# Kernel tuning notes

Hardware: AMD Instinct MI355X
Metric: run time of the kernel (lower is better)

The kernel has to match this reference:

```python
import jax, jax.numpy as jnp
import numpy as np

EPS = 1e-5
NUM_HEADS = 16
TEMP = 0.01

def _ln(x, g, b):
    m = jnp.mean(x, axis=-1, keepdims=True)
    v = jnp.var(x, axis=-1, keepdims=True)
    return (x - m) * jax.lax.rsqrt(v + EPS) * g + b

def setup_inputs() -> dict:
    key = jax.random.key(0)
    ks = jax.random.split(key, 16)
    b, l, c, ni = 4, 1024, 1024, 2
    d = c // NUM_HEADS
    s = lambda fan: 1.0 / np.sqrt(fan)
    return {
        "x_list": jax.random.normal(ks[0], (b, l, c, ni), jnp.float32),
        "w_": jax.random.normal(ks[1], (4 + ni, 1), jnp.float32),
        "qkv_w": jax.random.normal(ks[2], (3 * c, c), jnp.float32) * s(c),
        "qkv_b": jax.random.normal(ks[3], (3 * c,), jnp.float32) * 0.02,
        "proj_w": jax.random.normal(ks[4], (c, c), jnp.float32) * s(c),
        "proj_b": jax.random.normal(ks[5], (c,), jnp.float32) * 0.02,
        "nq_g": jnp.ones((d,), jnp.float32),
        "nq_b": jnp.zeros((d,), jnp.float32),
        "nk_g": jnp.ones((d,), jnp.float32),
        "nk_b": jnp.zeros((d,), jnp.float32),
        "conv_w": jax.random.normal(ks[6], (c, c), jnp.float32) * s(c),
        "conv_b": jax.random.normal(ks[7], (c,), jnp.float32) * 0.02,
        "ca1_w": jax.random.normal(ks[8], (c // 16, c), jnp.float32) * s(c),
        "ca1_b": jax.random.normal(ks[9], (c // 16,), jnp.float32) * 0.02,
        "ca2_w": jax.random.normal(ks[10], (c, c // 16), jnp.float32) * s(c // 16),
        "ca2_b": jax.random.normal(ks[11], (c,), jnp.float32) * 0.02,
        "mlp1_w": jax.random.normal(ks[12], (4 * c, c), jnp.float32) * s(c),
        "mlp1_b": jax.random.normal(ks[13], (4 * c,), jnp.float32) * 0.02,
        "mlp2_w": jax.random.normal(ks[14], (c, 4 * c), jnp.float32) * s(4 * c),
        "mlp2_b": jax.random.normal(ks[15], (c,), jnp.float32) * 0.02,
    }

def reference(x_list, w_, qkv_w, qkv_b, proj_w, proj_b, nq_g, nq_b, nk_g, nk_b,
              conv_w, conv_b, ca1_w, ca1_b, ca2_w, ca2_b, mlp1_w, mlp1_b, mlp2_w, mlp2_b):
    x = x_list[..., -1]  # [b, l, c]
    # op 0: Conv1x1Act = GELU(Linear)
    op0 = jax.nn.gelu(x @ conv_w.T + conv_b, approximate=False)
    # op 1: ChannelAttention = sigmoid(fc2(relu(fc1(x)))) * x
    op1 = jax.nn.sigmoid(jax.nn.relu(x @ ca1_w.T + ca1_b) @ ca2_w.T + ca2_b) * x
    # op 2: Identity
    op2 = x
    # op 3: MLP = fc2(GELU(fc1(x)))
    op3 = jax.nn.gelu(x @ mlp1_w.T + mlp1_b, approximate=False) @ mlp2_w.T + mlp2_b
    new = jnp.stack([op0, op1, op2, op3], axis=-1)  # [b, l, c, 4]
    xc = jnp.concatenate([x_list, new], axis=-1)    # [b, l, c, ni+4]
    w = jax.nn.softmax(w_ / TEMP, axis=0)           # [ni+4, 1]
    x = jnp.einsum('blcn,ni->blci', xc, w)[..., 0]  # [b, l, c]
    x_res = x
    # attention with per-head LayerNorm on q, k
    b_, n, c = x.shape
    d = c // NUM_HEADS
    qkv = x @ qkv_w.T + qkv_b
    q, k, v = jnp.split(qkv, 3, axis=-1)
    to_heads = lambda t: t.reshape(b_, n, NUM_HEADS, d).transpose(0, 2, 1, 3)  # [b, h, n, d]
    q, k, v = to_heads(q), to_heads(k), to_heads(v)
    q = _ln(q, nq_g, nq_b)
    k = _ln(k, nk_g, nk_b)
    score = jnp.einsum('bhnd,bhmd->bhnm', q, k) / np.sqrt(d).astype(np.float32)
    attn = jax.nn.softmax(score, axis=-1)           # [b, h, n, n]
    attn_map = attn.mean(axis=1)[:, 0, 1:]          # [b, n-1]
    out = jnp.einsum('bhnm,bhmd->bhnd', attn, v)
    out = out.transpose(0, 2, 1, 3).reshape(b_, n, c)
    out = out @ proj_w.T + proj_b + x_res
    return out, attn_map
```

## Files before the change

kernel.cpp:

```cpp
#include <hip/hip_runtime.h>
#include <hip/hip_bf16.h>

typedef __attribute__((ext_vector_type(8))) short short8;
typedef __attribute__((ext_vector_type(4))) float f32x4;

#define MROWS 4096
#define CDIM  1024
#define HEADS 16
#define DHEAD 64
#define NSEQ  1024

__device__ inline float softw(const float* __restrict__ w, int idx) {
    float m = w[0];
#pragma unroll
    for (int i = 1; i < 6; i++) m = fmaxf(m, w[i]);
    float s = 0.f, v = 0.f;
#pragma unroll
    for (int i = 0; i < 6; i++) {
        float e = __expf((w[i] - m) * 100.0f);
        s += e;
        if (i == idx) v = e;
    }
    return v / s;
}

__device__ inline float gelu_f(float x) {
    return 0.5f * x * (1.0f + erff(x * 0.70710678118654752f));
}

__global__ __launch_bounds__(256) void mix_base(
    const float* __restrict__ x_list, __hip_bfloat16* __restrict__ xb,
    float* __restrict__ am_acc)
{
    int i = blockIdx.x * 256 + threadIdx.x;
    xb[i] = __float2bfloat16(x_list[2 * (size_t)i + 1]);
    if (i < 4096) am_acc[i] = 0.f;
}

__global__ __launch_bounds__(256) void f2b(const float* __restrict__ in,
                                           __hip_bfloat16* __restrict__ out, int n)
{
    int i = blockIdx.x * 256 + threadIdx.x;
    if (i < n) out[i] = __float2bfloat16(in[i]);
}

#define BKT 32
#define LDA 40

template<int EPI, int FM, int FN>
__global__ __launch_bounds__(256) void gemm_bf16(
    const __hip_bfloat16* __restrict__ A, const __hip_bfloat16* __restrict__ W,
    const float* __restrict__ bias,
    float* __restrict__ f0, const float* __restrict__ f1,
    __hip_bfloat16* __restrict__ b0, __hip_bfloat16* __restrict__ b1,
    __hip_bfloat16* __restrict__ b2,
    const float* __restrict__ g0, const float* __restrict__ be0,
    const float* __restrict__ g1, const float* __restrict__ be1,
    const float* __restrict__ wvec, int M, int N, int K)
{
    constexpr int BMt = FM * 32;
    constexpr int BNt = FN * 32;
    constexpr int NA = BMt / 64;
    constexpr int NB = BNt / 64;
    __shared__ __hip_bfloat16 As[2][BMt * LDA];
    __shared__ __hip_bfloat16 Bs[2][BNt * LDA];
    int t = threadIdx.x;
    int n0 = blockIdx.x * BNt, m0 = blockIdx.y * BMt;
    int wave = t >> 6, lane = t & 63;
    int wr = wave >> 1, wc = wave & 1;
    int quad = lane >> 4, l16 = lane & 15;
    int r0 = t >> 2, c0 = (t & 3) * 8;

    short8 sa0[NA], sb0[NB], sa1[NA], sb1[NB];
    auto ldg = [&](int k0, short8* da, short8* db) {
#pragma unroll
        for (int i = 0; i < NA; i++)
            da[i] = *(const short8*)(A + (size_t)(m0 + r0 + 64 * i) * K + k0 + c0);
#pragma unroll
        for (int i = 0; i < NB; i++)
            db[i] = *(const short8*)(W + (size_t)(n0 + r0 + 64 * i) * K + k0 + c0);
    };
    ldg(0, sa0, sb0);
    ldg(BKT, sa1, sb1);

    f32x4 zero = {0.f, 0.f, 0.f, 0.f};
    f32x4 acc[FM][FN];
#pragma unroll
    for (int i = 0; i < FM; i++)
#pragma unroll
        for (int j = 0; j < FN; j++) acc[i][j] = zero;

    for (int k0 = 0; k0 < K; k0 += 2 * BKT) {
#pragma unroll
        for (int i = 0; i < NA; i++)
            *(short8*)&As[0][(r0 + 64 * i) * LDA + c0] = sa0[i];
#pragma unroll
        for (int i = 0; i < NB; i++)
            *(short8*)&Bs[0][(r0 + 64 * i) * LDA + c0] = sb0[i];
        __syncthreads();
        if (k0 + 2 * BKT < K) ldg(k0 + 2 * BKT, sa0, sb0);
        {
            short8 af[FM], bf[FN];
#pragma unroll
            for (int i = 0; i < FM; i++)
                af[i] = *(const short8*)&As[0][(wr * FM * 16 + i * 16 + l16) * LDA + quad * 8];
#pragma unroll
            for (int j = 0; j < FN; j++)
                bf[j] = *(const short8*)&Bs[0][(wc * FN * 16 + j * 16 + l16) * LDA + quad * 8];
#pragma unroll
            for (int i = 0; i < FM; i++)
#pragma unroll
                for (int j = 0; j < FN; j++)
                    acc[i][j] = __builtin_amdgcn_mfma_f32_16x16x32_bf16(
                        af[i], bf[j], acc[i][j], 0, 0, 0);
        }
#pragma unroll
        for (int i = 0; i < NA; i++)
            *(short8*)&As[1][(r0 + 64 * i) * LDA + c0] = sa1[i];
#pragma unroll
        for (int i = 0; i < NB; i++)
            *(short8*)&Bs[1][(r0 + 64 * i) * LDA + c0] = sb1[i];
        __syncthreads();
        if (k0 + 3 * BKT < K) ldg(k0 + 3 * BKT, sa1, sb1);
        {
            short8 af[FM], bf[FN];
#pragma unroll
            for (int i = 0; i < FM; i++)
                af[i] = *(const short8*)&As[1][(wr * FM * 16 + i * 16 + l16) * LDA + quad * 8];
#pragma unroll
            for (int j = 0; j < FN; j++)
                bf[j] = *(const short8*)&Bs[1][(wc * FN * 16 + j * 16 + l16) * LDA + quad * 8];
#pragma unroll
            for (int i = 0; i < FM; i++)
#pragma unroll
                for (int j = 0; j < FN; j++)
                    acc[i][j] = __builtin_amdgcn_mfma_f32_16x16x32_bf16(
                        af[i], bf[j], acc[i][j], 0, 0, 0);
        }
    }

    if constexpr (EPI == 1) {
        float wmx = softw(wvec, 2);
        float w0c = softw(wvec, 0);
        float w14c = softw(wvec, 1) + softw(wvec, 4);
        int colbase = n0 + wc * FN * 16;
        bool isconv = colbase < 1024;
#pragma unroll
        for (int i = 0; i < FM; i++) {
#pragma unroll
            for (int j = 0; j < FN; j++) {
                int col = colbase + j * 16 + l16;
                float bv = isconv ? bias[col] : be0[col - 1024];
#pragma unroll
                for (int r = 0; r < 4; r++) {
                    int row = m0 + wr * FM * 16 + i * 16 + quad * 4 + r;
                    float v = acc[i][j][r] + bv;
                    if (isconv) {
                        size_t idx = (size_t)row * 1024 + col;
                        float2 xl = ((const float2*)f1)[idx];
                        b0[idx] = __float2bfloat16(
                            w0c * xl.x + w14c * xl.y + wmx * gelu_f(v));
                    } else {
                        b1[(size_t)row * 4096 + (col - 1024)] =
                            __float2bfloat16(gelu_f(v));
                    }
                }
            }
        }
        return;
    }

    if constexpr (EPI == 5) {
        int colbase = n0 + wc * FN * 16;
        int portion = colbase >> 10;
        int hh = (colbase >> 6) & 15;
        float bv[FN];
#pragma unroll
        for (int j = 0; j < FN; j++) bv[j] = bias[colbase + j * 16 + l16];
        if (portion == 2) {
#pragma unroll
            for (int i = 0; i < FM; i++)
#pragma unroll
                for (int j = 0; j < FN; j++)
#pragma unroll
                    for (int r = 0; r < 4; r++) {
                        int row = m0 + wr * FM * 16 + i * 16 + quad * 4 + r;
                        int bb = row >> 10, nn = row & 1023;
                        int dd = j * 16 + l16;
                        b0[((size_t)(bb * 16 + hh) * DHEAD + dd) * NSEQ + nn] =
                            __float2bfloat16(acc[i][j][r] + bv[j]);
                    }
        } else {
            const float* g  = (portion == 0) ? g0 : g1;
            const float* be = (portion == 0) ? be0 : be1;
            __hip_bfloat16* dst = (portion == 0) ? b1 : b2;
            float gv[FN], bev[FN];
#pragma unroll
            for (int j = 0; j < FN; j++) {
                gv[j] = g[j * 16 + l16];
                bev[j] = be[j * 16 + l16];
            }
#pragma unroll
            for (int i = 0; i < FM; i++)
#pragma unroll
                for (int r = 0; r < 4; r++) {
                    float s1 = 0.f, s2 = 0.f;
#pragma unroll
                    for (int j = 0; j < FN; j++) {
                        float v = acc[i][j][r] + bv[j];
                        s1 += v; s2 += v * v;
                    }
#pragma unroll
                    for (int mk = 1; mk < 16; mk <<= 1) {
                        s1 += __shfl_xor(s1, mk, 64);
                        s2 += __shfl_xor(s2, mk, 64);
                    }
                    float mean = s1 * (1.f / 64.f);
                    float var = s2 * (1.f / 64.f) - mean * mean;
                    float rs = rsqrtf(var + 1e-5f);
                    int row = m0 + wr * FM * 16 + i * 16 + quad * 4 + r;
                    int bb = row >> 10, nn = row & 1023;
                    size_t base = ((size_t)(bb * 16 + hh) * NSEQ + nn) * DHEAD;
#pragma unroll
                    for (int j = 0; j < FN; j++)
                        dst[base + j * 16 + l16] = __float2bfloat16(
                            (acc[i][j][r] + bv[j] - mean) * rs * gv[j] + bev[j]);
                }
        }
        return;
    }

    float wmx = 0.f;
    if (EPI == 3) wmx = softw(wvec, 5);

#pragma unroll
    for (int i = 0; i < FM; i++) {
#pragma unroll
        for (int j = 0; j < FN; j++) {
            int col = n0 + wc * FN * 16 + j * 16 + l16;
            float bv = bias[col];
#pragma unroll
            for (int r = 0; r < 4; r++) {
                int row = m0 + wr * FM * 16 + i * 16 + quad * 4 + r;
                float v = acc[i][j][r] + bv;
                size_t idx = (size_t)row * N + col;
                if (EPI == 3) {
                    float tv = __bfloat162float(b0[idx]) + wmx * v;
                    b0[idx] = __float2bfloat16(tv);
                } else if (EPI == 4) {
                    f0[idx] = v + __bfloat162float(b1[idx]);
                }
            }
        }
    }
}

__global__ __launch_bounds__(256) void ca1_kernel(
    const __hip_bfloat16* __restrict__ xb, const float* __restrict__ w,
    const float* __restrict__ bias, float* __restrict__ h1)
{
    __shared__ float Xs[16 * 65];
    __shared__ float Ws[64 * 65];
    int t = threadIdx.x;
    int m0 = blockIdx.x * 16;
    int row = t >> 4, cg = t & 15;
    float acc[4] = {0.f, 0.f, 0.f, 0.f};
    for (int k0 = 0; k0 < 1024; k0 += 64) {
#pragma unroll
        for (int i = 0; i < 4; i++) {
            int e = t + i * 256; int r = e >> 6, c = e & 63;
            Xs[r * 65 + c] = __bfloat162float(xb[(size_t)(m0 + r) * 1024 + k0 + c]);
        }
#pragma unroll
        for (int i = 0; i < 16; i++) {
            int e = t + i * 256; int r = e >> 6, c = e & 63;
            Ws[r * 65 + c] = w[(size_t)r * 1024 + k0 + c];
        }
        __syncthreads();
        for (int k = 0; k < 64; k++) {
            float xv = Xs[row * 65 + k];
#pragma unroll
            for (int c = 0; c < 4; c++)
                acc[c] += xv * Ws[(cg * 4 + c) * 65 + k];
        }
        __syncthreads();
    }
#pragma unroll
    for (int c = 0; c < 4; c++)
        h1[(size_t)(m0 + row) * 64 + cg * 4 + c] =
            fmaxf(acc[c] + bias[cg * 4 + c], 0.f);
}

__global__ __launch_bounds__(256) void ca2_kernel(
    const float* __restrict__ h1, const float* __restrict__ w,
    const float* __restrict__ bias, const __hip_bfloat16* __restrict__ xb,
    __hip_bfloat16* __restrict__ xmixb, const float* __restrict__ wvec)
{
    __shared__ float Wt[256 * 65];
    __shared__ float hs[16 * 64];
    int t = threadIdx.x;
    int m0 = blockIdx.x * 16, n0 = blockIdx.y * 256;
#pragma unroll
    for (int i = 0; i < 64; i++) {
        int e = t + i * 256; int r = e >> 6, c = e & 63;
        Wt[r * 65 + c] = w[(size_t)(n0 + r) * 64 + c];
    }
#pragma unroll
    for (int i = 0; i < 4; i++) {
        int e = t + i * 256; int r = e >> 6, c = e & 63;
        hs[r * 64 + c] = h1[(size_t)(m0 + r) * 64 + c];
    }
    __syncthreads();
    int n = n0 + t;
    float bv = bias[n];
    float acc[16];
#pragma unroll
    for (int mi = 0; mi < 16; mi++) acc[mi] = bv;
    for (int k = 0; k < 64; k++) {
        float wv = Wt[t * 65 + k];
#pragma unroll
        for (int mi = 0; mi < 16; mi++) acc[mi] += hs[mi * 64 + k] * wv;
    }
    float w3 = softw(wvec, 3);
#pragma unroll
    for (int mi = 0; mi < 16; mi++) {
        size_t idx = (size_t)(m0 + mi) * 1024 + n;
        float sg = 1.f / (1.f + __expf(-acc[mi]));
        float cur = __bfloat162float(xmixb[idx]);
        xmixb[idx] = __float2bfloat16(cur + w3 * sg * __bfloat162float(xb[idx]));
    }
}

#define PSTR 72
__global__ __launch_bounds__(256) void flash_mfma(
    const __hip_bfloat16* __restrict__ qb, const __hip_bfloat16* __restrict__ kb,
    const __hip_bfloat16* __restrict__ vt, __hip_bfloat16* __restrict__ ao)
{
    __shared__ __hip_bfloat16 Plds[4][32 * PSTR];
    int bh = blockIdx.x;
    int i0 = blockIdx.y * 128;
    int b = bh >> 4, h = bh & 15;
    int t = threadIdx.x, wave = t >> 6, lane = t & 63;
    int l16 = lane & 15, quad = lane >> 4;
    const __hip_bfloat16* qbase = qb + (size_t)bh * NSEQ * DHEAD;
    const __hip_bfloat16* kbase = kb + (size_t)bh * NSEQ * DHEAD;
    const __hip_bfloat16* vbase = vt + (size_t)bh * DHEAD * NSEQ;
    __hip_bfloat16* pw = Plds[wave];
    int qrow0 = i0 + wave * 32;

    short8 aq[2][2];
#pragma unroll
    for (int ri = 0; ri < 2; ri++)
#pragma unroll
        for (int ks = 0; ks < 2; ks++)
            aq[ri][ks] = *(const short8*)(qbase +
                (size_t)(qrow0 + ri * 16 + l16) * DHEAD + ks * 32 + quad * 8);

    f32x4 zero = {0.f, 0.f, 0.f, 0.f};
    f32x4 o[2][4];
    float mrow[2][4], lrow[2][4];
#pragma unroll
    for (int ri = 0; ri < 2; ri++) {
#pragma unroll
        for (int nt = 0; nt < 4; nt++) o[ri][nt] = zero;
#pragma unroll
        for (int rr = 0; rr < 4; rr++) { mrow[ri][rr] = -1e30f; lrow[ri][rr] = 0.f; }
    }

    for (int j0 = 0; j0 < NSEQ; j0 += 64) {
        short8 bk[4][2];
#pragma unroll
        for (int jt = 0; jt < 4; jt++)
#pragma unroll
            for (int ks = 0; ks < 2; ks++)
                bk[jt][ks] = *(const short8*)(kbase +
                    (size_t)(j0 + jt * 16 + l16) * DHEAD + ks * 32 + quad * 8);
        short8 bv[4][2];
#pragma unroll
        for (int nt = 0; nt < 4; nt++)
#pragma unroll
            for (int ks = 0; ks < 2; ks++)
                bv[nt][ks] = *(const short8*)(vbase +
                    (size_t)(nt * 16 + l16) * NSEQ + j0 + ks * 32 + quad * 8);

#pragma unroll
        for (int ri = 0; ri < 2; ri++) {
            f32x4 s[4];
#pragma unroll
            for (int jt = 0; jt < 4; jt++) s[jt] = zero;
#pragma unroll
            for (int jt = 0; jt < 4; jt++)
#pragma unroll
                for (int ks = 0; ks < 2; ks++)
                    s[jt] = __builtin_amdgcn_mfma_f32_16x16x32_bf16(
                        aq[ri][ks], bk[jt][ks], s[jt], 0, 0, 0);
#pragma unroll
            for (int rr = 0; rr < 4; rr++) {
                float mx = -1e30f;
#pragma unroll
                for (int jt = 0; jt < 4; jt++) {
                    s[jt][rr] *= 0.125f;
                    mx = fmaxf(mx, s[jt][rr]);
                }
#pragma unroll
                for (int mk = 1; mk < 16; mk <<= 1) mx = fmaxf(mx, __shfl_xor(mx, mk, 64));
                float om = mrow[ri][rr];
                float nm = fmaxf(om, mx);
                float al = __expf(om - nm);
                mrow[ri][rr] = nm;
                float ss = 0.f;
#pragma unroll
                for (int jt = 0; jt < 4; jt++) {
                    float p = __expf(s[jt][rr] - nm);
                    pw[(ri * 16 + quad * 4 + rr) * PSTR + jt * 16 + l16] =
                        __float2bfloat16(p);
                    ss += p;
                }
#pragma unroll
                for (int mk = 1; mk < 16; mk <<= 1) ss += __shfl_xor(ss, mk, 64);
                lrow[ri][rr] = lrow[ri][rr] * al + ss;
#pragma unroll
                for (int nt = 0; nt < 4; nt++) o[ri][nt][rr] *= al;
            }
        }
#pragma unroll
        for (int ri = 0; ri < 2; ri++) {
            short8 ap[2];
#pragma unroll
            for (int ks = 0; ks < 2; ks++)
                ap[ks] = *(const short8*)&pw[(ri * 16 + l16) * PSTR + ks * 32 + quad * 8];
#pragma unroll
            for (int nt = 0; nt < 4; nt++)
#pragma unroll
                for (int ks = 0; ks < 2; ks++)
                    o[ri][nt] = __builtin_amdgcn_mfma_f32_16x16x32_bf16(
                        ap[ks], bv[nt][ks], o[ri][nt], 0, 0, 0);
        }
    }

#pragma unroll
    for (int ri = 0; ri < 2; ri++)
#pragma unroll
        for (int rr = 0; rr < 4; rr++) {
            float inv = 1.f / lrow[ri][rr];
            int row = qrow0 + ri * 16 + quad * 4 + rr;
#pragma unroll
            for (int nt = 0; nt < 4; nt++)
                ao[((size_t)b * NSEQ + row) * CDIM + h * 64 + nt * 16 + l16] =
                    __float2bfloat16(o[ri][nt][rr] * inv);
        }
}

__global__ __launch_bounds__(256) void attn_map_acc(
    const __hip_bfloat16* __restrict__ qf, const __hip_bfloat16* __restrict__ kf,
    float* __restrict__ am)
{
    __shared__ float q0[64];
    __shared__ float red[256];
    int bh = blockIdx.x, t = threadIdx.x;
    const __hip_bfloat16* qr = qf + (size_t)bh * NSEQ * DHEAD;
    const __hip_bfloat16* kb = kf + (size_t)bh * NSEQ * DHEAD;
    if (t < 64) q0[t] = __bfloat162float(qr[t]);
    __syncthreads();
    float s[4];
    float mx = -1e30f;
#pragma unroll
    for (int ji = 0; ji < 4; ji++) {
        int j = ji * 256 + t;
        float a = 0.f;
        for (int k = 0; k < 64; k++) a += q0[k] * __bfloat162float(kb[(size_t)j * 64 + k]);
        a *= 0.125f;
        s[ji] = a;
        mx = fmaxf(mx, a);
    }
    red[t] = mx; __syncthreads();
    for (int st = 128; st > 0; st >>= 1) {
        if (t < st) red[t] = fmaxf(red[t], red[t + st]);
        __syncthreads();
    }
    float M = red[0]; __syncthreads();
    float sum = 0.f;
#pragma unroll
    for (int ji = 0; ji < 4; ji++) { s[ji] = __expf(s[ji] - M); sum += s[ji]; }
    red[t] = sum; __syncthreads();
    for (int st = 128; st > 0; st >>= 1) {
        if (t < st) red[t] += red[t + st];
        __syncthreads();
    }
    float inv = 1.f / red[0];
    int b = bh >> 4;
#pragma unroll
    for (int ji = 0; ji < 4; ji++) {
        int j = ji * 256 + t;
        if (j > 0) atomicAdd(&am[b * 1024 + j], s[ji] * inv * (1.f / 16.f));
    }
}

__global__ __launch_bounds__(256) void attn_map_out(
    const float* __restrict__ am, float* __restrict__ out1)
{
    int i = blockIdx.x * 256 + threadIdx.x;
    if (i < 4 * 1023) {
        int b = i / 1023;
        int j = i - b * 1023 + 1;
        out1[i] = am[b * 1024 + j];
    }
}

extern "C" void kernel_launch(void* const* d_in, const int* in_sizes, int n_in,
                              void* d_out, int out_size, void* d_ws, size_t ws_size,
                              hipStream_t stream)
{
    const float* x_list = (const float*)d_in[0];
    const float* wvec   = (const float*)d_in[1];
    const float* qkv_w  = (const float*)d_in[2];
    const float* qkv_b  = (const float*)d_in[3];
    const float* proj_w = (const float*)d_in[4];
    const float* proj_b = (const float*)d_in[5];
    const float* nq_g   = (const float*)d_in[6];
    const float* nq_b   = (const float*)d_in[7];
    const float* nk_g   = (const float*)d_in[8];
    const float* nk_b   = (const float*)d_in[9];
    const float* conv_w = (const float*)d_in[10];
    const float* conv_b = (const float*)d_in[11];
    const float* ca1_w  = (const float*)d_in[12];
    const float* ca1_b  = (const float*)d_in[13];
    const float* ca2_w  = (const float*)d_in[14];
    const float* ca2_b  = (const float*)d_in[15];
    const float* mlp1_w = (const float*)d_in[16];
    const float* mlp1_b = (const float*)d_in[17];
    const float* mlp2_w = (const float*)d_in[18];
    const float* mlp2_b = (const float*)d_in[19];

    float* out0 = (float*)d_out;
    float* out1 = out0 + (size_t)4 * 1024 * 1024;

    char* ws = (char*)d_ws;
    size_t off = 0;
    auto alloc = [&](size_t bytes) -> char* {
        char* p = ws + off;
        off += (bytes + 255) & ~(size_t)255;
        return p;
    };
    __hip_bfloat16* xb     = (__hip_bfloat16*)alloc((size_t)MROWS * CDIM * 2);
    __hip_bfloat16* xmixb  = (__hip_bfloat16*)alloc((size_t)MROWS * CDIM * 2);
    float*          h1     = (float*)alloc((size_t)MROWS * 64 * 4);
    __hip_bfloat16* hb     = (__hip_bfloat16*)alloc((size_t)MROWS * 4096 * 2);
    __hip_bfloat16* qbb    = (__hip_bfloat16*)alloc((size_t)MROWS * CDIM * 2);
    __hip_bfloat16* kbb    = (__hip_bfloat16*)alloc((size_t)MROWS * CDIM * 2);
    __hip_bfloat16* vtb    = (__hip_bfloat16*)alloc((size_t)MROWS * CDIM * 2);
    __hip_bfloat16* aob    = (__hip_bfloat16*)alloc((size_t)MROWS * CDIM * 2);
    float*          amacc  = (float*)alloc(4096 * 4);
    __hip_bfloat16* wcat   = (__hip_bfloat16*)alloc((size_t)5120 * 1024 * 2);
    __hip_bfloat16* qkvwb  = (__hip_bfloat16*)alloc((size_t)3145728 * 2);
    __hip_bfloat16* projwb = (__hip_bfloat16*)alloc((size_t)1048576 * 2);
    __hip_bfloat16* mlp2wb = (__hip_bfloat16*)alloc((size_t)4194304 * 2);

    f2b<<<4096, 256, 0, stream>>>(conv_w, wcat, 1048576);
    f2b<<<16384, 256, 0, stream>>>(mlp1_w, wcat + (size_t)1048576, 4194304);
    f2b<<<12288, 256, 0, stream>>>(qkv_w, qkvwb, 3145728);
    f2b<<<4096, 256, 0, stream>>>(proj_w, projwb, 1048576);
    f2b<<<16384, 256, 0, stream>>>(mlp2_w, mlp2wb, 4194304);

    mix_base<<<16384, 256, 0, stream>>>(x_list, xb, amacc);

    gemm_bf16<1, 4, 4><<<dim3(40, 32), 256, 0, stream>>>(
        xb, wcat, conv_b, nullptr, x_list, xmixb, hb, nullptr,
        nullptr, mlp1_b, nullptr, nullptr, wvec, MROWS, 5120, 1024);

    ca1_kernel<<<256, 256, 0, stream>>>(xb, ca1_w, ca1_b, h1);
    ca2_kernel<<<dim3(256, 4), 256, 0, stream>>>(h1, ca2_w, ca2_b, xb, xmixb, wvec);

    gemm_bf16<3, 4, 4><<<dim3(8, 32), 256, 0, stream>>>(
        hb, mlp2wb, mlp2_b, nullptr, nullptr, xmixb, nullptr, nullptr,
        nullptr, nullptr, nullptr, nullptr, wvec, MROWS, 1024, 4096);

    gemm_bf16<5, 4, 4><<<dim3(24, 32), 256, 0, stream>>>(
        xmixb, qkvwb, qkv_b, nullptr, nullptr, vtb, qbb, kbb,
        nq_g, nq_b, nk_g, nk_b, wvec, MROWS, 3072, 1024);

    flash_mfma<<<dim3(64, 8), 256, 0, stream>>>(qbb, kbb, vtb, aob);

    attn_map_acc<<<64, 256, 0, stream>>>(qbb, kbb, amacc);
    attn_map_out<<<16, 256, 0, stream>>>(amacc, out1);

    gemm_bf16<4, 4, 4><<<dim3(8, 32), 256, 0, stream>>>(
        aob, projwb, proj_b, out0, nullptr, nullptr, xmixb, nullptr,
        nullptr, nullptr, nullptr, nullptr, wvec, MROWS, 1024, 1024);
}
```

Before: 549.6 us.

## Add 256x256 direct-to-LDS GEMM for fused conv/mlp1 and QKV; merge weight casts

Adds a new 512-thread GEMM kernel with 256x256 tiles that loads A and B straight into a 4-stage shared-memory ring via global_load_lds. It uses swizzled addressing, XCD-aware block remapping, split barriers and MFMA priority hints. It replaces the 128x128 GEMM for the conv+mlp1 and QKV projections. It also merges the five weight-cast launches into one vectorized kernel and vectorizes the input extraction. The aim is more data reuse per tile, fewer launches and better load/compute overlap. The cost is heavy register and LDS use, with only 320 or 192 blocks, so fewer blocks are available to fill the CUs.

```diff
diff --git a/kernel.cpp b/kernel.cpp
--- a/kernel.cpp
+++ b/kernel.cpp
@@ -32,16 +32,35 @@
     const float* __restrict__ x_list, __hip_bfloat16* __restrict__ xb,
     float* __restrict__ am_acc)
 {
-    int i = blockIdx.x * 256 + threadIdx.x;
-    xb[i] = __float2bfloat16(x_list[2 * (size_t)i + 1]);
-    if (i < 4096) am_acc[i] = 0.f;
-}
-
-__global__ __launch_bounds__(256) void f2b(const float* __restrict__ in,
-                                           __hip_bfloat16* __restrict__ out, int n)
-{
-    int i = blockIdx.x * 256 + threadIdx.x;
-    if (i < n) out[i] = __float2bfloat16(in[i]);
+    int i2 = blockIdx.x * 256 + threadIdx.x;
+    float4 v = ((const float4*)x_list)[i2];
+    __hip_bfloat162 o;
+    o.x = __float2bfloat16(v.y);
+    o.y = __float2bfloat16(v.w);
+    ((__hip_bfloat162*)xb)[i2] = o;
+    if (i2 < 4096) am_acc[i2] = 0.f;
+}
+
+__global__ __launch_bounds__(256) void f2b_all(
+    const float* __restrict__ conv_w, const float* __restrict__ mlp1_w,
+    const float* __restrict__ qkv_w, const float* __restrict__ proj_w,
+    const float* __restrict__ mlp2_w,
+    __hip_bfloat16* __restrict__ wcat, __hip_bfloat16* __restrict__ qkvwb,
+    __hip_bfloat16* __restrict__ projwb, __hip_bfloat16* __restrict__ mlp2wb)
+{
+    size_t e = ((size_t)blockIdx.x * 256 + threadIdx.x) * 4;
+    const float* src; __hip_bfloat16* dst; size_t o;
+    if (e < 1048576)       { src = conv_w; dst = wcat;           o = e; }
+    else if (e < 5242880)  { src = mlp1_w; dst = wcat + 1048576; o = e - 1048576; }
+    else if (e < 8388608)  { src = qkv_w;  dst = qkvwb;          o = e - 5242880; }
+    else if (e < 9437184)  { src = proj_w; dst = projwb;         o = e - 8388608; }
+    else                   { src = mlp2_w; dst = mlp2wb;         o = e - 9437184; }
+    float4 v = *(const float4*)(src + o);
+    __hip_bfloat162 a, b;
+    a.x = __float2bfloat16(v.x); a.y = __float2bfloat16(v.y);
+    b.x = __float2bfloat16(v.z); b.y = __float2bfloat16(v.w);
+    *(__hip_bfloat162*)(dst + o)     = a;
+    *(__hip_bfloat162*)(dst + o + 2) = b;
 }
 
 #define BKT 32
@@ -139,22 +158,147 @@
         }
     }
 
+    float wmx = 0.f;
+    if (EPI == 3) wmx = softw(wvec, 5);
+
+#pragma unroll
+    for (int i = 0; i < FM; i++) {
+#pragma unroll
+        for (int j = 0; j < FN; j++) {
+            int col = n0 + wc * FN * 16 + j * 16 + l16;
+            float bv = bias[col];
+#pragma unroll
+            for (int r = 0; r < 4; r++) {
+                int row = m0 + wr * FM * 16 + i * 16 + quad * 4 + r;
+                float v = acc[i][j][r] + bv;
+                size_t idx = (size_t)row * N + col;
+                if (EPI == 3) {
+                    float tv = __bfloat162float(b0[idx]) + wmx * v;
+                    b0[idx] = __float2bfloat16(tv);
+                } else if (EPI == 4) {
+                    f0[idx] = v + __bfloat162float(b1[idx]);
+                }
+            }
+        }
+    }
+}
+
+template<int EPI>
+__global__ __launch_bounds__(512, 2) void gemm8(
+    const __hip_bfloat16* __restrict__ A, const __hip_bfloat16* __restrict__ W,
+    const float* __restrict__ bias,
+    float* __restrict__ f0, const float* __restrict__ f1,
+    __hip_bfloat16* __restrict__ b0, __hip_bfloat16* __restrict__ b1,
+    __hip_bfloat16* __restrict__ b2,
+    const float* __restrict__ g0, const float* __restrict__ be0,
+    const float* __restrict__ g1, const float* __restrict__ be1,
+    const float* __restrict__ wvec, int M, int N, int K, int NT)
+{
+    __shared__ __hip_bfloat16 As[4][256 * 32];
+    __shared__ __hip_bfloat16 Bs[4][256 * 32];
+    int t = threadIdx.x;
+    int w = t >> 6, lane = t & 63;
+    int quad = lane >> 4, l16 = lane & 15;
+    int wr = w >> 2, wc = w & 3;
+
+    int qq = gridDim.x >> 3;
+    int wg = (blockIdx.x & 7) * qq + (blockIdx.x >> 3);
+    int n0 = (wg % NT) << 8, m0 = (wg / NT) << 8;
+
+    int srow = w * 16 + (lane >> 2);
+    int scol = ((lane & 3) ^ ((lane >> 2) & 3)) * 8;
+    const __hip_bfloat16* pa = A + (size_t)(m0 + srow) * K + scol;
+    const __hip_bfloat16* pb = W + (size_t)(n0 + srow) * K + scol;
+    int ldso = w * 512;
+
+    auto stageA = [&](int s) {
+        int sl = s & 3; int k0 = s << 5;
+#pragma unroll
+        for (int i = 0; i < 2; i++)
+            __builtin_amdgcn_global_load_lds(
+                (const __attribute__((address_space(1))) void*)(pa + (size_t)i * 128 * K + k0),
+                (__attribute__((address_space(3))) void*)(&As[sl][i * 4096 + ldso]),
+                16, 0, 0);
+    };
+    auto stageB = [&](int s) {
+        int sl = s & 3; int k0 = s << 5;
+#pragma unroll
+        for (int i = 0; i < 2; i++)
+            __builtin_amdgcn_global_load_lds(
+                (const __attribute__((address_space(1))) void*)(pb + (size_t)i * 128 * K + k0),
+                (__attribute__((address_space(3))) void*)(&Bs[sl][i * 4096 + ldso]),
+                16, 0, 0);
+    };
+
+    int arow = wr * 128 + l16;
+    int brow = wc * 64 + l16;
+    int aswz = (quad ^ (l16 & 3)) * 8;
+
+    f32x4 zero = {0.f, 0.f, 0.f, 0.f};
+    f32x4 acc[8][4];
+#pragma unroll
+    for (int i = 0; i < 8; i++)
+#pragma unroll
+        for (int j = 0; j < 4; j++) acc[i][j] = zero;
+
+    int S = K >> 5;
+    stageA(0); stageB(0); stageA(1); stageB(1);
+
+    for (int s = 0; s < S; s++) {
+        int sl = s & 3;
+        if (s + 2 < S) stageA(s + 2);
+        if (s + 2 < S)      asm volatile("s_waitcnt vmcnt(6)" ::: "memory");
+        else if (s + 1 < S) asm volatile("s_waitcnt vmcnt(4)" ::: "memory");
+        else                asm volatile("s_waitcnt vmcnt(0)" ::: "memory");
+        asm volatile("s_barrier" ::: "memory");
+
+        short8 af[4], bf[4], af2[4];
+#pragma unroll
+        for (int mi = 0; mi < 4; mi++)
+            af[mi] = *(const short8*)&As[sl][(arow + mi * 16) * 32 + aswz];
+#pragma unroll
+        for (int ni = 0; ni < 4; ni++)
+            bf[ni] = *(const short8*)&Bs[sl][(brow + ni * 16) * 32 + aswz];
+        __builtin_amdgcn_s_setprio(1);
+#pragma unroll
+        for (int mi = 0; mi < 4; mi++)
+#pragma unroll
+            for (int ni = 0; ni < 4; ni++)
+                acc[mi][ni] = __builtin_amdgcn_mfma_f32_16x16x32_bf16(
+                    af[mi], bf[ni], acc[mi][ni], 0, 0, 0);
+        __builtin_amdgcn_s_setprio(0);
+
+#pragma unroll
+        for (int mi = 0; mi < 4; mi++)
+            af2[mi] = *(const short8*)&As[sl][(arow + (mi + 4) * 16) * 32 + aswz];
+        if (s + 2 < S) stageB(s + 2);
+        asm volatile("s_barrier" ::: "memory");
+        __builtin_amdgcn_s_setprio(1);
+#pragma unroll
+        for (int mi = 0; mi < 4; mi++)
+#pragma unroll
+            for (int ni = 0; ni < 4; ni++)
+                acc[mi + 4][ni] = __builtin_amdgcn_mfma_f32_16x16x32_bf16(
+                    af2[mi], bf[ni], acc[mi + 4][ni], 0, 0, 0);
+        __builtin_amdgcn_s_setprio(0);
+    }
+
     if constexpr (EPI == 1) {
         float wmx = softw(wvec, 2);
         float w0c = softw(wvec, 0);
         float w14c = softw(wvec, 1) + softw(wvec, 4);
-        int colbase = n0 + wc * FN * 16;
+        int colbase = n0 + wc * 64;
         bool isconv = colbase < 1024;
 #pragma unroll
-        for (int i = 0; i < FM; i++) {
-#pragma unroll
-            for (int j = 0; j < FN; j++) {
-                int col = colbase + j * 16 + l16;
+        for (int mi = 0; mi < 8; mi++) {
+#pragma unroll
+            for (int ni = 0; ni < 4; ni++) {
+                int col = colbase + ni * 16 + l16;
                 float bv = isconv ? bias[col] : be0[col - 1024];
 #pragma unroll
                 for (int r = 0; r < 4; r++) {
-                    int row = m0 + wr * FM * 16 + i * 16 + quad * 4 + r;
-                    float v = acc[i][j][r] + bv;
+                    int row = m0 + wr * 128 + mi * 16 + quad * 4 + r;
+                    float v = acc[mi][ni][r] + bv;
                     if (isconv) {
                         size_t idx = (size_t)row * 1024 + col;
                         float2 xl = ((const float2*)f1)[idx];
@@ -171,43 +315,43 @@
     }
 
     if constexpr (EPI == 5) {
-        int colbase = n0 + wc * FN * 16;
+        int colbase = n0 + wc * 64;
         int portion = colbase >> 10;
         int hh = (colbase >> 6) & 15;
-        float bv[FN];
-#pragma unroll
-        for (int j = 0; j < FN; j++) bv[j] = bias[colbase + j * 16 + l16];
+        float bv[4];
+#pragma unroll
+        for (int ni = 0; ni < 4; ni++) bv[ni] = bias[colbase + ni * 16 + l16];
         if (portion == 2) {
 #pragma unroll
-            for (int i = 0; i < FM; i++)
-#pragma unroll
-                for (int j = 0; j < FN; j++)
+            for (int mi = 0; mi < 8; mi++)
+#pragma unroll
+                for (int ni = 0; ni < 4; ni++)
 #pragma unroll
                     for (int r = 0; r < 4; r++) {
-                        int row = m0 + wr * FM * 16 + i * 16 + quad * 4 + r;
+                        int row = m0 + wr * 128 + mi * 16 + quad * 4 + r;
                         int bb = row >> 10, nn = row & 1023;
-                        int dd = j * 16 + l16;
+                        int dd = ni * 16 + l16;
                         b0[((size_t)(bb * 16 + hh) * DHEAD + dd) * NSEQ + nn] =
-                            __float2bfloat16(acc[i][j][r] + bv[j]);
+                            __float2bfloat16(acc[mi][ni][r] + bv[ni]);
                     }
         } else {
             const float* g  = (portion == 0) ? g0 : g1;
             const float* be = (portion == 0) ? be0 : be1;
             __hip_bfloat16* dst = (portion == 0) ? b1 : b2;
-            float gv[FN], bev[FN];
-#pragma unroll
-            for (int j = 0; j < FN; j++) {
-                gv[j] = g[j * 16 + l16];
-                bev[j] = be[j * 16 + l16];
+            float gv[4], bev[4];
+#pragma unroll
+            for (int ni = 0; ni < 4; ni++) {
+                gv[ni] = g[ni * 16 + l16];
+                bev[ni] = be[ni * 16 + l16];
             }
 #pragma unroll
-            for (int i = 0; i < FM; i++)
+            for (int mi = 0; mi < 8; mi++)
 #pragma unroll
                 for (int r = 0; r < 4; r++) {
                     float s1 = 0.f, s2 = 0.f;
 #pragma unroll
-                    for (int j = 0; j < FN; j++) {
-                        float v = acc[i][j][r] + bv[j];
+                    for (int ni = 0; ni < 4; ni++) {
+                        float v = acc[mi][ni][r] + bv[ni];
                         s1 += v; s2 += v * v;
                     }
 #pragma unroll
@@ -218,40 +362,16 @@
                     float mean = s1 * (1.f / 64.f);
                     float var = s2 * (1.f / 64.f) - mean * mean;
                     float rs = rsqrtf(var + 1e-5f);
-                    int row = m0 + wr * FM * 16 + i * 16 + quad * 4 + r;
+                    int row = m0 + wr * 128 + mi * 16 + quad * 4 + r;
                     int bb = row >> 10, nn = row & 1023;
                     size_t base = ((size_t)(bb * 16 + hh) * NSEQ + nn) * DHEAD;
 #pragma unroll
-                    for (int j = 0; j < FN; j++)
-                        dst[base + j * 16 + l16] = __float2bfloat16(
-                            (acc[i][j][r] + bv[j] - mean) * rs * gv[j] + bev[j]);
+                    for (int ni = 0; ni < 4; ni++)
+                        dst[base + ni * 16 + l16] = __float2bfloat16(
+                            (acc[mi][ni][r] + bv[ni] - mean) * rs * gv[ni] + bev[ni]);
                 }
         }
         return;
-    }
-
-    float wmx = 0.f;
-    if (EPI == 3) wmx = softw(wvec, 5);
-
-#pragma unroll
-    for (int i = 0; i < FM; i++) {
-#pragma unroll
-        for (int j = 0; j < FN; j++) {
-            int col = n0 + wc * FN * 16 + j * 16 + l16;
-            float bv = bias[col];
-#pragma unroll
-            for (int r = 0; r < 4; r++) {
-                int row = m0 + wr * FM * 16 + i * 16 + quad * 4 + r;
-                float v = acc[i][j][r] + bv;
-                size_t idx = (size_t)row * N + col;
-                if (EPI == 3) {
-                    float tv = __bfloat162float(b0[idx]) + wmx * v;
-                    b0[idx] = __float2bfloat16(tv);
-                } else if (EPI == 4) {
-                    f0[idx] = v + __bfloat162float(b1[idx]);
-                }
-            }
-        }
     }
 }
 
@@ -556,17 +676,14 @@
     __hip_bfloat16* projwb = (__hip_bfloat16*)alloc((size_t)1048576 * 2);
     __hip_bfloat16* mlp2wb = (__hip_bfloat16*)alloc((size_t)4194304 * 2);
 
-    f2b<<<4096, 256, 0, stream>>>(conv_w, wcat, 1048576);
-    f2b<<<16384, 256, 0, stream>>>(mlp1_w, wcat + (size_t)1048576, 4194304);
-    f2b<<<12288, 256, 0, stream>>>(qkv_w, qkvwb, 3145728);
-    f2b<<<4096, 256, 0, stream>>>(proj_w, projwb, 1048576);
-    f2b<<<16384, 256, 0, stream>>>(mlp2_w, mlp2wb, 4194304);
-
-    mix_base<<<16384, 256, 0, stream>>>(x_list, xb, amacc);
-
-    gemm_bf16<1, 4, 4><<<dim3(40, 32), 256, 0, stream>>>(
+    f2b_all<<<13312, 256, 0, stream>>>(conv_w, mlp1_w, qkv_w, proj_w, mlp2_w,
+                                       wcat, qkvwb, projwb, mlp2wb);
+
+    mix_base<<<8192, 256, 0, stream>>>(x_list, xb, amacc);
+
+    gemm8<1><<<320, 512, 0, stream>>>(
         xb, wcat, conv_b, nullptr, x_list, xmixb, hb, nullptr,
-        nullptr, mlp1_b, nullptr, nullptr, wvec, MROWS, 5120, 1024);
+        nullptr, mlp1_b, nullptr, nullptr, wvec, MROWS, 5120, 1024, 20);
 
     ca1_kernel<<<256, 256, 0, stream>>>(xb, ca1_w, ca1_b, h1);
     ca2_kernel<<<dim3(256, 4), 256, 0, stream>>>(h1, ca2_w, ca2_b, xb, xmixb, wvec);
@@ -575,9 +692,9 @@
         hb, mlp2wb, mlp2_b, nullptr, nullptr, xmixb, nullptr, nullptr,
         nullptr, nullptr, nullptr, nullptr, wvec, MROWS, 1024, 4096);
 
-    gemm_bf16<5, 4, 4><<<dim3(24, 32), 256, 0, stream>>>(
+    gemm8<5><<<192, 512, 0, stream>>>(
         xmixb, qkvwb, qkv_b, nullptr, nullptr, vtb, qbb, kbb,
-        nq_g, nq_b, nk_g, nk_b, wvec, MROWS, 3072, 1024);
+        nq_g, nq_b, nk_g, nk_b, wvec, MROWS, 3072, 1024, 12);
 
     flash_mfma<<<dim3(64, 8), 256, 0, stream>>>(qbb, kbb, vtb, aob);
 
```

New measurement: 571.4 us. +4.0%, slower.
